# Performance work log

Hardware: AMD Instinct MI355X
Metric: run time of the kernel (lower is better)

## Reference

```python
import jax, jax.numpy as jnp
import numpy as np

GRID = (32, 32, 32)  # must match init grid_size


def setup_inputs() -> dict:
    key = jax.random.key(0)
    # Mimic the module's init: D = 0.01 everywhere + 0.1 on the 6x6 diagonal,
    # plus small uniform noise so the baseline exercises non-degenerate values.
    D = jax.random.uniform(key, (6, 6, *GRID), dtype=jnp.float32) * 0.02 + 0.01
    D = D.at[jnp.arange(6), jnp.arange(6)].add(0.1)
    return {"D": D, "sx": 1, "sy": 1, "sz": 1, "ex": 30, "ey": 30, "ez": 30,
            "max_iterations": 300}


def reference(D, sx, sy, sz, ex, ey, ez, max_iterations):
    """flash_wave (training path, inference=False): 300-step CA as one lax.scan.

    Returns the stacked history of phi (pre-update, as the torch loop appends
    phi at the top of each iteration): shape [max_iterations, 6, X, Y, Z].
    Early exit is emulated by freezing phi once the wave reaches (ex,ey,ez),
    so no per-step host sync is needed.
    """
    phi0 = jnp.zeros((6, *GRID), dtype=D.dtype).at[:, sx, sy, sz].set(1.0)
    active_D = D + 0.95  # inference=False branch

    def body(carry, _):
        phi, done = carry
        # 6x6 channel mixing per grid cell: 'oixyz,ixyz->oxyz'
        phi_out = jnp.einsum('oixyz,ixyz->oxyz', active_D, phi)
        pn = jnp.zeros_like(phi)
        pn = pn.at[0, 1:, :, :].set(phi_out[0, :-1, :, :])   # +x
        pn = pn.at[1, :-1, :, :].set(phi_out[1, 1:, :, :])   # -x
        pn = pn.at[2, :, 1:, :].set(phi_out[2, :, :-1, :])   # +y
        pn = pn.at[3, :, :-1, :].set(phi_out[3, :, 1:, :])   # -y
        pn = pn.at[4, :, :, 1:].set(phi_out[4, :, :, :-1])   # +z
        pn = pn.at[5, :, :, :-1].set(phi_out[5, :, :, 1:])   # -z
        nxt = jnp.clip(pn, 0.0, 1.0)
        nxt = jnp.where(done, phi, nxt)  # freeze after target reached
        reached = jnp.sum(nxt[:, ex, ey, ez]) > 0.01
        return (nxt, jnp.logical_or(done, reached)), phi

    (_, _), history = jax.lax.scan(body, (phi0, jnp.array(False)), None,
                                   length=int(max_iterations))
    return history
```

## Files before the change

kernel.cpp:

```cpp
#include <hip/hip_runtime.h>

#define NCH 6
#define NX 32
#define PLANE 1024
#define NCELL (NX * PLANE)
#define STEP_STRIDE (NCH * NCELL)
#define NTHREADS 256
#define NBLOCKS 128
#define RB 2

#define RING_WORDS ((size_t)RB * 3 * NCELL)
#define F_DONE 0

typedef unsigned long long u64;
typedef float fx4 __attribute__((ext_vector_type(4)));

__device__ __forceinline__ u64 ld64(const u64* p) {
    return __hip_atomic_load(p, __ATOMIC_RELAXED, __HIP_MEMORY_SCOPE_AGENT);
}
__device__ __forceinline__ void st64(u64* p, u64 v) {
    __hip_atomic_store(p, v, __ATOMIC_RELAXED, __HIP_MEMORY_SCOPE_AGENT);
}
__device__ __forceinline__ int ldi(const int* p) {
    return __hip_atomic_load(p, __ATOMIC_RELAXED, __HIP_MEMORY_SCOPE_AGENT);
}
__device__ __forceinline__ void sti(int* p, int v) {
    __hip_atomic_store(p, v, __ATOMIC_RELAXED, __HIP_MEMORY_SCOPE_AGENT);
}
__device__ __forceinline__ u64 pack2p(float a, float b, unsigned P) {
    const u64 w = ((u64)__float_as_uint(b) << 32) | __float_as_uint(a);
    return P ? (w | 0x8000000080000000ULL) : w;
}
__device__ __forceinline__ bool tagok(u64 w, unsigned P) {
    return (((unsigned)(w >> 63)) == P) & ((((unsigned)w) >> 31) == P);
}
__device__ __forceinline__ void unpack2(u64 w, float* d0, float* d1) {
    *d0 = __uint_as_float((unsigned)w & 0x7fffffffu);
    *d1 = __uint_as_float((unsigned)(w >> 32) & 0x7fffffffu);
}

__global__ void __launch_bounds__(NTHREADS)
BEMNA_V7_2_PhaseSpace_44117904064519_kernel(
    const float* __restrict__ D,
    const int* __restrict__ sx_p, const int* __restrict__ sy_p,
    const int* __restrict__ sz_p, const int* __restrict__ ex_p,
    const int* __restrict__ ey_p, const int* __restrict__ ez_p,
    const int* __restrict__ maxit_p,
    float* __restrict__ out,
    u64* __restrict__ ring,
    int* __restrict__ flags)
{
    __shared__ float tile[2][NCH][NTHREADS];
    __shared__ int lds_dn;

    const int tid = (int)threadIdx.x;
    const int bx  = (int)blockIdx.x;
    const int x   = bx >> 2;
    const int s   = bx & 3;
    const int yl  = tid >> 5;
    const int z   = tid & 31;
    const int y   = (s << 3) + yl;
    const int cell = (x << 10) + (y << 5) + z;

    const int sx = *sx_p, sy = *sy_p, sz = *sz_p;
    const int ex = *ex_p, ey = *ey_p, ez = *ez_p;
    const int maxit = *maxit_p;
    const bool is_seed   = (cell == ((sx << 10) | (sy << 5) | sz));
    const bool is_target = (cell == ((ex << 10) | (ey << 5) | ez));

    const int  nbg[NCH] = { cell - PLANE, cell + PLANE, cell - 32, cell + 32, cell - 1, cell + 1 };
    const bool ok[NCH]  = { x >= 1, x <= 30, y >= 1, y <= 30, z >= 1, z <= 30 };
    const int izm = (tid - 1) & (NTHREADS - 1), izp = (tid + 1) & (NTHREADS - 1);

    const bool has_xm = (x >= 1), has_xp = (x <= 30);
    const bool has_ym = (yl == 0) && (y >= 1);
    const bool has_yp = (yl == 7) && (y <= 30);

    float dreg[NCH][NCH];
#pragma unroll
    for (int o = 0; o < NCH; ++o)
#pragma unroll
        for (int i = 0; i < NCH; ++i)
            dreg[o][i] = ok[o] ? D[(size_t)(o * NCH + i) * NCELL + nbg[o]] + 0.95f : 0.0f;

    const float iv = is_seed ? 1.0f : 0.0f;
    {
        const u64 p = pack2p(iv, iv, 0);
        st64(&ring[0 * NCELL + cell], p);
        st64(&ring[1 * NCELL + cell], p);
        st64(&ring[2 * NCELL + cell], p);
        float* outp = out + cell;
#pragma unroll
        for (int o = 0; o < NCH; ++o) {
            __builtin_nontemporal_store(iv, outp + o * NCELL);
            tile[0][o][tid] = iv;
        }
    }
    __syncthreads();

    int tripped = 0;
    for (int t = 0; t <= maxit - 2; ++t) {
        const u64* r0 = ring + (size_t)(t & 1) * 3 * NCELL;
        const u64* r1 = r0 + NCELL;
        const u64* r2 = r1 + NCELL;
        const unsigned P = (unsigned)((t >> 1) & 1);
        const int cm = cell - PLANE, cp = cell + PLANE;
        const int am = cell - 32,    ap = cell + 32;

        u64 wa0 = 0, wa1 = 0, wa2 = 0, wb0 = 0, wb1 = 0, wb2 = 0;
        u64 wc0 = 0, wc1 = 0, wc2 = 0, wd0 = 0, wd1 = 0, wd2 = 0;
        int dn = -1, spins = 0;
        for (;;) {
            if (has_xm) { wa0 = ld64(r0 + cm); wa1 = ld64(r1 + cm); wa2 = ld64(r2 + cm); }
            if (has_xp) { wb0 = ld64(r0 + cp); wb1 = ld64(r1 + cp); wb2 = ld64(r2 + cp); }
            if (has_ym) { wc0 = ld64(r0 + am); wc1 = ld64(r1 + am); wc2 = ld64(r2 + am); }
            if (has_yp) { wd0 = ld64(r0 + ap); wd1 = ld64(r1 + ap); wd2 = ld64(r2 + ap); }
            dn = ldi(&flags[F_DONE]);
            bool okr = true;
            if (has_xm) okr = okr & tagok(wa0, P) & tagok(wa1, P) & tagok(wa2, P);
            if (has_xp) okr = okr & tagok(wb0, P) & tagok(wb1, P) & tagok(wb2, P);
            if (has_ym) okr = okr & tagok(wc0, P) & tagok(wc1, P) & tagok(wc2, P);
            if (has_yp) okr = okr & tagok(wd0, P) & tagok(wd1, P) & tagok(wd2, P);
            if (dn >= 0 && t + 1 > dn) break;
            if (__ballot(okr) == ~0ull) break;
            if (spins++) __builtin_amdgcn_s_sleep(1);
        }
        if (tid == 0) lds_dn = dn;
        __syncthreads();
        if (lds_dn >= 0 && t + 1 > lds_dn) break;

        float xm[NCH], xp[NCH], ym[NCH], yp[NCH];
        unpack2(wa0, &xm[0], &xm[1]); unpack2(wa1, &xm[2], &xm[3]); unpack2(wa2, &xm[4], &xm[5]);
        unpack2(wb0, &xp[0], &xp[1]); unpack2(wb1, &xp[2], &xp[3]); unpack2(wb2, &xp[4], &xp[5]);
        unpack2(wc0, &ym[0], &ym[1]); unpack2(wc1, &ym[2], &ym[3]); unpack2(wc2, &ym[4], &ym[5]);
        unpack2(wd0, &yp[0], &yp[1]); unpack2(wd1, &yp[2], &yp[3]); unpack2(wd2, &yp[4], &yp[5]);

        const float (*L)[NTHREADS] = tile[t & 1];
        if (!has_ym) {
            const int n = (tid - 32) & (NTHREADS - 1);
#pragma unroll
            for (int i = 0; i < NCH; ++i) ym[i] = L[i][n];
        }
        if (!has_yp) {
            const int n = (tid + 32) & (NTHREADS - 1);
#pragma unroll
            for (int i = 0; i < NCH; ++i) yp[i] = L[i][n];
        }

        float v[NCH];
        {
            float a0 = 0.f, a1 = 0.f, a2 = 0.f, a3 = 0.f, a4 = 0.f, a5 = 0.f;
#pragma unroll
            for (int i = 0; i < NCH; ++i) {
                a0 = fmaf(dreg[0][i], xm[i], a0);
                a1 = fmaf(dreg[1][i], xp[i], a1);
                a2 = fmaf(dreg[2][i], ym[i], a2);
                a3 = fmaf(dreg[3][i], yp[i], a3);
                a4 = fmaf(dreg[4][i], L[i][izm], a4);
                a5 = fmaf(dreg[5][i], L[i][izp], a5);
            }
            v[0] = fminf(fmaxf(a0, 0.f), 1.f);
            v[1] = fminf(fmaxf(a1, 0.f), 1.f);
            v[2] = fminf(fmaxf(a2, 0.f), 1.f);
            v[3] = fminf(fmaxf(a3, 0.f), 1.f);
            v[4] = fminf(fmaxf(a4, 0.f), 1.f);
            v[5] = fminf(fmaxf(a5, 0.f), 1.f);
        }

        if (is_target && !tripped) {
            if (v[0] + v[1] + v[2] + v[3] + v[4] + v[5] > 0.01f) {
                sti(&flags[F_DONE], t + 1);
                tripped = 1;
            }
        }

        {
            const unsigned P1 = (unsigned)(((t + 1) >> 1) & 1);
            u64* w0 = ring + (size_t)((t + 1) & 1) * 3 * NCELL;
            st64(w0 + 0 * NCELL + cell, pack2p(v[0], v[1], P1));
            st64(w0 + 1 * NCELL + cell, pack2p(v[2], v[3], P1));
            st64(w0 + 2 * NCELL + cell, pack2p(v[4], v[5], P1));
#pragma unroll
            for (int o = 0; o < NCH; ++o) tile[(t + 1) & 1][o][tid] = v[o];
        }

        {
            float* outp = out + (size_t)(t + 1) * STEP_STRIDE + cell;
#pragma unroll
            for (int o = 0; o < NCH; ++o)
                __builtin_nontemporal_store(v[o], outp + o * NCELL);
        }
    }
}

__global__ void fill_kernel(const int* __restrict__ flags,
                            float* __restrict__ outf,
                            int total4)
{
    const int s4 = STEP_STRIDE / 4;
    const int maxit = total4 / s4;
    const int ds = flags[F_DONE];
    const int tf = (ds >= 1 && ds <= maxit - 1) ? ds : maxit - 1;
    const int idx = (int)blockIdx.x * (int)blockDim.x + (int)threadIdx.x;
    fx4* o4 = (fx4*)outf;
    const fx4 v = o4[(size_t)tf * s4 + idx];
    for (int t = tf + 1; t < maxit; ++t)
        __builtin_nontemporal_store(v, &o4[(size_t)t * s4 + idx]);
}

extern "C" void kernel_launch(void* const* d_in, const int* in_sizes, int n_in,
                              void* d_out, int out_size, void* d_ws, size_t ws_size,
                              hipStream_t stream)
{
    const float* D   = (const float*)d_in[0];
    const int* sx    = (const int*)d_in[1];
    const int* sy    = (const int*)d_in[2];
    const int* sz    = (const int*)d_in[3];
    const int* ex    = (const int*)d_in[4];
    const int* ey    = (const int*)d_in[5];
    const int* ez    = (const int*)d_in[6];
    const int* maxit = (const int*)d_in[7];
    float* out = (float*)d_out;

    u64* ring  = (u64*)d_ws;
    int* flags = (int*)(ring + RING_WORDS);

    BEMNA_V7_2_PhaseSpace_44117904064519_kernel<<<dim3(NBLOCKS), dim3(NTHREADS), 0, stream>>>(
        D, sx, sy, sz, ex, ey, ez, maxit, out, ring, flags);

    const int total4 = out_size / 4;
    fill_kernel<<<dim3((STEP_STRIDE / 4) / 256), dim3(256), 0, stream>>>(
        flags, out, total4);
}
```

Measured before the change: 401.9 us.

## Exchange mixed per-direction outputs instead of full phi vectors between blocks

Restructures the step so each cell computes its 6x6 mix locally and publishes only the single directional output each neighbour needs, rather than neighbours reading all six phi channels and mixing with neighbour-indexed D. Inter-block ring traffic drops from three 64-bit words per neighbour to one 32-bit tagged word, y-direction boundary stores are limited to edge rows, and z-neighbours come via wave shuffles instead of LDS. The aim is to cut the latency and bandwidth of the per-step spin-wait exchange. Sign-bit tagging now relies on the mixed values being non-negative before clamping.

```diff
diff --git a/kernel.cpp b/kernel.cpp
--- a/kernel.cpp
+++ b/kernel.cpp
@@ -9,16 +9,17 @@
 #define NBLOCKS 128
 #define RB 2
 
-#define RING_WORDS ((size_t)RB * 3 * NCELL)
+#define RING32_WORDS ((size_t)RB * 4 * NCELL)
 #define F_DONE 0
 
 typedef unsigned long long u64;
+typedef unsigned int u32;
 typedef float fx4 __attribute__((ext_vector_type(4)));
 
-__device__ __forceinline__ u64 ld64(const u64* p) {
+__device__ __forceinline__ u32 ld32(const u32* p) {
     return __hip_atomic_load(p, __ATOMIC_RELAXED, __HIP_MEMORY_SCOPE_AGENT);
 }
-__device__ __forceinline__ void st64(u64* p, u64 v) {
+__device__ __forceinline__ void st32(u32* p, u32 v) {
     __hip_atomic_store(p, v, __ATOMIC_RELAXED, __HIP_MEMORY_SCOPE_AGENT);
 }
 __device__ __forceinline__ int ldi(const int* p) {
@@ -27,16 +28,12 @@
 __device__ __forceinline__ void sti(int* p, int v) {
     __hip_atomic_store(p, v, __ATOMIC_RELAXED, __HIP_MEMORY_SCOPE_AGENT);
 }
-__device__ __forceinline__ u64 pack2p(float a, float b, unsigned P) {
-    const u64 w = ((u64)__float_as_uint(b) << 32) | __float_as_uint(a);
-    return P ? (w | 0x8000000080000000ULL) : w;
-}
-__device__ __forceinline__ bool tagok(u64 w, unsigned P) {
-    return (((unsigned)(w >> 63)) == P) & ((((unsigned)w) >> 31) == P);
-}
-__device__ __forceinline__ void unpack2(u64 w, float* d0, float* d1) {
-    *d0 = __uint_as_float((unsigned)w & 0x7fffffffu);
-    *d1 = __uint_as_float((unsigned)(w >> 32) & 0x7fffffffu);
+__device__ __forceinline__ u32 tagf(float a, unsigned P) {
+    const u32 w = __float_as_uint(a);
+    return P ? (w | 0x80000000u) : w;
+}
+__device__ __forceinline__ float untagf(u32 w) {
+    return __uint_as_float(w & 0x7fffffffu);
 }
 
 __global__ void __launch_bounds__(NTHREADS)
@@ -47,10 +44,10 @@
     const int* __restrict__ ey_p, const int* __restrict__ ez_p,
     const int* __restrict__ maxit_p,
     float* __restrict__ out,
-    u64* __restrict__ ring,
+    u32* __restrict__ ring,
     int* __restrict__ flags)
 {
-    __shared__ float tile[2][NCH][NTHREADS];
+    __shared__ float tile[2][2][NTHREADS];
     __shared__ int lds_dn;
 
     const int tid = (int)threadIdx.x;
@@ -68,59 +65,63 @@
     const bool is_seed   = (cell == ((sx << 10) | (sy << 5) | sz));
     const bool is_target = (cell == ((ex << 10) | (ey << 5) | ez));
 
-    const int  nbg[NCH] = { cell - PLANE, cell + PLANE, cell - 32, cell + 32, cell - 1, cell + 1 };
-    const bool ok[NCH]  = { x >= 1, x <= 30, y >= 1, y <= 30, z >= 1, z <= 30 };
-    const int izm = (tid - 1) & (NTHREADS - 1), izp = (tid + 1) & (NTHREADS - 1);
-
-    const bool has_xm = (x >= 1), has_xp = (x <= 30);
-    const bool has_ym = (yl == 0) && (y >= 1);
-    const bool has_yp = (yl == 7) && (y <= 30);
-
     float dreg[NCH][NCH];
 #pragma unroll
     for (int o = 0; o < NCH; ++o)
 #pragma unroll
         for (int i = 0; i < NCH; ++i)
-            dreg[o][i] = ok[o] ? D[(size_t)(o * NCH + i) * NCELL + nbg[o]] + 0.95f : 0.0f;
+            dreg[o][i] = D[(size_t)(o * NCH + i) * NCELL + cell] + 0.95f;
+
+    const bool has_xm  = (x >= 1), has_xp = (x <= 30);
+    const bool edge_ym = (yl == 0), edge_yp = (yl == 7);
+    const bool has_ym  = edge_ym && (y >= 1);
+    const bool has_yp  = edge_yp && (y <= 30);
+    const bool pub_d2  = edge_yp && (y <= 30);
+    const bool pub_d3  = edge_ym && (y >= 1);
 
     const float iv = is_seed ? 1.0f : 0.0f;
+    float pz4, pz5;
     {
-        const u64 p = pack2p(iv, iv, 0);
-        st64(&ring[0 * NCELL + cell], p);
-        st64(&ring[1 * NCELL + cell], p);
-        st64(&ring[2 * NCELL + cell], p);
+        float po[NCH];
+#pragma unroll
+        for (int o = 0; o < NCH; ++o) {
+            float a = 0.f;
+#pragma unroll
+            for (int i = 0; i < NCH; ++i) a = fmaf(dreg[o][i], iv, a);
+            po[o] = a;
+        }
+        st32(ring + 0 * NCELL + cell, tagf(po[0], 0));
+        st32(ring + 1 * NCELL + cell, tagf(po[1], 0));
+        if (pub_d2) st32(ring + 2 * NCELL + cell, tagf(po[2], 0));
+        if (pub_d3) st32(ring + 3 * NCELL + cell, tagf(po[3], 0));
+        tile[0][0][tid] = po[2];
+        tile[0][1][tid] = po[3];
+        pz4 = po[4]; pz5 = po[5];
         float* outp = out + cell;
 #pragma unroll
-        for (int o = 0; o < NCH; ++o) {
+        for (int o = 0; o < NCH; ++o)
             __builtin_nontemporal_store(iv, outp + o * NCELL);
-            tile[0][o][tid] = iv;
-        }
     }
     __syncthreads();
 
     int tripped = 0;
     for (int t = 0; t <= maxit - 2; ++t) {
-        const u64* r0 = ring + (size_t)(t & 1) * 3 * NCELL;
-        const u64* r1 = r0 + NCELL;
-        const u64* r2 = r1 + NCELL;
+        const u32* r = ring + (size_t)(t & 1) * 4 * NCELL;
         const unsigned P = (unsigned)((t >> 1) & 1);
-        const int cm = cell - PLANE, cp = cell + PLANE;
-        const int am = cell - 32,    ap = cell + 32;
-
-        u64 wa0 = 0, wa1 = 0, wa2 = 0, wb0 = 0, wb1 = 0, wb2 = 0;
-        u64 wc0 = 0, wc1 = 0, wc2 = 0, wd0 = 0, wd1 = 0, wd2 = 0;
+
+        u32 wxm = 0, wxp = 0, wym = 0, wyp = 0;
         int dn = -1, spins = 0;
         for (;;) {
-            if (has_xm) { wa0 = ld64(r0 + cm); wa1 = ld64(r1 + cm); wa2 = ld64(r2 + cm); }
-            if (has_xp) { wb0 = ld64(r0 + cp); wb1 = ld64(r1 + cp); wb2 = ld64(r2 + cp); }
-            if (has_ym) { wc0 = ld64(r0 + am); wc1 = ld64(r1 + am); wc2 = ld64(r2 + am); }
-            if (has_yp) { wd0 = ld64(r0 + ap); wd1 = ld64(r1 + ap); wd2 = ld64(r2 + ap); }
+            if (has_xm) wxm = ld32(r + 0 * NCELL + cell - PLANE);
+            if (has_xp) wxp = ld32(r + 1 * NCELL + cell + PLANE);
+            if (has_ym) wym = ld32(r + 2 * NCELL + cell - 32);
+            if (has_yp) wyp = ld32(r + 3 * NCELL + cell + 32);
             dn = ldi(&flags[F_DONE]);
             bool okr = true;
-            if (has_xm) okr = okr & tagok(wa0, P) & tagok(wa1, P) & tagok(wa2, P);
-            if (has_xp) okr = okr & tagok(wb0, P) & tagok(wb1, P) & tagok(wb2, P);
-            if (has_ym) okr = okr & tagok(wc0, P) & tagok(wc1, P) & tagok(wc2, P);
-            if (has_yp) okr = okr & tagok(wd0, P) & tagok(wd1, P) & tagok(wd2, P);
+            if (has_xm) okr = okr & ((wxm >> 31) == P);
+            if (has_xp) okr = okr & ((wxp >> 31) == P);
+            if (has_ym) okr = okr & ((wym >> 31) == P);
+            if (has_yp) okr = okr & ((wyp >> 31) == P);
             if (dn >= 0 && t + 1 > dn) break;
             if (__ballot(okr) == ~0ull) break;
             if (spins++) __builtin_amdgcn_s_sleep(1);
@@ -129,43 +130,17 @@
         __syncthreads();
         if (lds_dn >= 0 && t + 1 > lds_dn) break;
 
-        float xm[NCH], xp[NCH], ym[NCH], yp[NCH];
-        unpack2(wa0, &xm[0], &xm[1]); unpack2(wa1, &xm[2], &xm[3]); unpack2(wa2, &xm[4], &xm[5]);
-        unpack2(wb0, &xp[0], &xp[1]); unpack2(wb1, &xp[2], &xp[3]); unpack2(wb2, &xp[4], &xp[5]);
-        unpack2(wc0, &ym[0], &ym[1]); unpack2(wc1, &ym[2], &ym[3]); unpack2(wc2, &ym[4], &ym[5]);
-        unpack2(wd0, &yp[0], &yp[1]); unpack2(wd1, &yp[2], &yp[3]); unpack2(wd2, &yp[4], &yp[5]);
-
-        const float (*L)[NTHREADS] = tile[t & 1];
-        if (!has_ym) {
-            const int n = (tid - 32) & (NTHREADS - 1);
-#pragma unroll
-            for (int i = 0; i < NCH; ++i) ym[i] = L[i][n];
-        }
-        if (!has_yp) {
-            const int n = (tid + 32) & (NTHREADS - 1);
-#pragma unroll
-            for (int i = 0; i < NCH; ++i) yp[i] = L[i][n];
-        }
-
         float v[NCH];
-        {
-            float a0 = 0.f, a1 = 0.f, a2 = 0.f, a3 = 0.f, a4 = 0.f, a5 = 0.f;
-#pragma unroll
-            for (int i = 0; i < NCH; ++i) {
-                a0 = fmaf(dreg[0][i], xm[i], a0);
-                a1 = fmaf(dreg[1][i], xp[i], a1);
-                a2 = fmaf(dreg[2][i], ym[i], a2);
-                a3 = fmaf(dreg[3][i], yp[i], a3);
-                a4 = fmaf(dreg[4][i], L[i][izm], a4);
-                a5 = fmaf(dreg[5][i], L[i][izp], a5);
-            }
-            v[0] = fminf(fmaxf(a0, 0.f), 1.f);
-            v[1] = fminf(fmaxf(a1, 0.f), 1.f);
-            v[2] = fminf(fmaxf(a2, 0.f), 1.f);
-            v[3] = fminf(fmaxf(a3, 0.f), 1.f);
-            v[4] = fminf(fmaxf(a4, 0.f), 1.f);
-            v[5] = fminf(fmaxf(a5, 0.f), 1.f);
-        }
+        v[0] = has_xm ? untagf(wxm) : 0.0f;
+        v[1] = has_xp ? untagf(wxp) : 0.0f;
+        v[2] = edge_ym ? (has_ym ? untagf(wym) : 0.0f) : tile[t & 1][0][tid - 32];
+        v[3] = edge_yp ? (has_yp ? untagf(wyp) : 0.0f) : tile[t & 1][1][tid + 32];
+        const float s4 = __shfl_up(pz4, 1, 32);
+        const float s5 = __shfl_down(pz5, 1, 32);
+        v[4] = (z >= 1)  ? s4 : 0.0f;
+        v[5] = (z <= 30) ? s5 : 0.0f;
+#pragma unroll
+        for (int o = 0; o < NCH; ++o) v[o] = fminf(fmaxf(v[o], 0.0f), 1.0f);
 
         if (is_target && !tripped) {
             if (v[0] + v[1] + v[2] + v[3] + v[4] + v[5] > 0.01f) {
@@ -174,14 +149,27 @@
             }
         }
 
+        float n0 = 0.f, n1 = 0.f, n2 = 0.f, n3 = 0.f, n4 = 0.f, n5 = 0.f;
+#pragma unroll
+        for (int i = 0; i < NCH; ++i) {
+            n0 = fmaf(dreg[0][i], v[i], n0);
+            n1 = fmaf(dreg[1][i], v[i], n1);
+            n2 = fmaf(dreg[2][i], v[i], n2);
+            n3 = fmaf(dreg[3][i], v[i], n3);
+            n4 = fmaf(dreg[4][i], v[i], n4);
+            n5 = fmaf(dreg[5][i], v[i], n5);
+        }
+
         {
             const unsigned P1 = (unsigned)(((t + 1) >> 1) & 1);
-            u64* w0 = ring + (size_t)((t + 1) & 1) * 3 * NCELL;
-            st64(w0 + 0 * NCELL + cell, pack2p(v[0], v[1], P1));
-            st64(w0 + 1 * NCELL + cell, pack2p(v[2], v[3], P1));
-            st64(w0 + 2 * NCELL + cell, pack2p(v[4], v[5], P1));
-#pragma unroll
-            for (int o = 0; o < NCH; ++o) tile[(t + 1) & 1][o][tid] = v[o];
+            u32* w = ring + (size_t)((t + 1) & 1) * 4 * NCELL;
+            st32(w + 0 * NCELL + cell, tagf(n0, P1));
+            st32(w + 1 * NCELL + cell, tagf(n1, P1));
+            if (pub_d2) st32(w + 2 * NCELL + cell, tagf(n2, P1));
+            if (pub_d3) st32(w + 3 * NCELL + cell, tagf(n3, P1));
+            tile[(t + 1) & 1][0][tid] = n2;
+            tile[(t + 1) & 1][1][tid] = n3;
+            pz4 = n4; pz5 = n5;
         }
 
         {
@@ -222,8 +210,8 @@
     const int* maxit = (const int*)d_in[7];
     float* out = (float*)d_out;
 
-    u64* ring  = (u64*)d_ws;
-    int* flags = (int*)(ring + RING_WORDS);
+    u32* ring  = (u32*)d_ws;
+    int* flags = (int*)(ring + RING32_WORDS);
 
     BEMNA_V7_2_PhaseSpace_44117904064519_kernel<<<dim3(NBLOCKS), dim3(NTHREADS), 0, stream>>>(
         D, sx, sy, sz, ex, ey, ez, maxit, out, ring, flags);
```

Result: faster. 348.1 us (median of 2 runs) (-13.4%).
